# Optimization experiments

Measured on AMD Instinct MI355X. Metric: run time of the kernel, lower is better.

## Reference

```python
import jax, jax.numpy as jnp
import numpy as np

EMBED_DIM = 512
NUM_HEADS = 8
HEAD_DIM = EMBED_DIM // NUM_HEADS
PAIR_BONUS = 2.0
MIN_SEPARATION = 3
PAIRING_MATRIX = jnp.array([
    [0, 1, 0, 0, 0],
    [1, 0, 1, 0, 0],
    [0, 1, 0, 1, 0],
    [0, 0, 1, 0, 0],
    [0, 0, 0, 0, 0],
], dtype=jnp.float32)


def setup_inputs() -> dict:
    key = jax.random.key(0)
    ks = jax.random.split(key, 12)
    B, S, E = 8, 1024, EMBED_DIM
    scale = 1.0 / np.sqrt(E)
    inp = {
        "query": jax.random.normal(ks[0], (B, S, E), dtype=jnp.float32),
        "key": jax.random.normal(ks[1], (B, S, E), dtype=jnp.float32),
        "value": jax.random.normal(ks[2], (B, S, E), dtype=jnp.float32),
        "nucleotide_sequence": jax.random.randint(ks[3], (B, S), 0, 5, dtype=jnp.int32),
        "key_padding_mask": jnp.zeros((B, S), dtype=bool),
        "Wq": jax.random.normal(ks[4], (E, E), dtype=jnp.float32) * scale,
        "bq": jnp.zeros((E,), dtype=jnp.float32),
        "Wk": jax.random.normal(ks[5], (E, E), dtype=jnp.float32) * scale,
        "bk": jnp.zeros((E,), dtype=jnp.float32),
        "Wv": jax.random.normal(ks[6], (E, E), dtype=jnp.float32) * scale,
        "bv": jnp.zeros((E,), dtype=jnp.float32),
        "Wo": jax.random.normal(ks[7], (E, E), dtype=jnp.float32) * scale,
        "bo": jnp.zeros((E,), dtype=jnp.float32),
    }
    return inp


def reference(query, key, value, nucleotide_sequence, key_padding_mask,
              Wq, bq, Wk, bk, Wv, bv, Wo, bo):
    B, T, E = query.shape
    S = key.shape[1]
    H, D = NUM_HEADS, HEAD_DIM
    scaling = D ** -0.5

    # projections -> (B, H, L, D)
    q = (query @ Wq + bq).reshape(B, T, H, D).transpose(0, 2, 1, 3)
    k = (key @ Wk + bk).reshape(B, S, H, D).transpose(0, 2, 1, 3)
    v = (value @ Wv + bv).reshape(B, S, H, D).transpose(0, 2, 1, 3)

    attn = jnp.einsum('bhtd,bhsd->bhts', q, k) * scaling  # (B,H,T,S)

    # base-pairing bias: gather into 5x5 table, masked by min separation
    pos = jnp.arange(S)
    sep_ok = (jnp.abs(pos[:, None] - pos[None, :]) >= MIN_SEPARATION).astype(jnp.float32)
    pairing = PAIRING_MATRIX[nucleotide_sequence[:, :, None], nucleotide_sequence[:, None, :]]  # (B,S,S)
    pair_bonus = pairing * sep_ok[None] * PAIR_BONUS
    attn = attn + pair_bonus[:, None, :, :]

    # key padding mask -> -inf
    attn = jnp.where(key_padding_mask[:, None, None, :], -jnp.inf, attn)

    attn_probs = jax.nn.softmax(attn, axis=-1)
    out = jnp.einsum('bhts,bhsd->bhtd', attn_probs, v)
    out = out.transpose(0, 2, 1, 3).reshape(B, T, E)
    out = out @ Wo + bo
    return out, attn_probs
```

## Files before the change

kernel.cpp:

```cpp
#include <hip/hip_runtime.h>
#include <hip/hip_bf16.h>
#include <stdint.h>


typedef float  f32x4  __attribute__((ext_vector_type(4)));
typedef short  s16x8  __attribute__((ext_vector_type(8)));

__device__ __forceinline__ ushort f2bf(float f) {
  union { float f; uint32_t u; } v; v.f = f;
  uint32_t u = v.u;
  return (ushort)((u + 0x7FFF + ((u >> 16) & 1)) >> 16);
}

__device__ __forceinline__ f32x4 mfma16(s16x8 a, s16x8 b, f32x4 c) {
  return __builtin_amdgcn_mfma_f32_16x16x32_bf16(a, b, c, 0, 0, 0);
}

__device__ __forceinline__ void gl_lds16(const void* g, void* l) {
  typedef __attribute__((address_space(1))) const void gvoid;
  typedef __attribute__((address_space(3))) void lvoid;
  __builtin_amdgcn_global_load_lds((gvoid*)(uintptr_t)g,
                                   (lvoid*)(uint32_t)(uintptr_t)l, 16, 0, 0);
}

__device__ __forceinline__ void vwait4() {
  asm volatile("s_waitcnt vmcnt(4)" ::: "memory");
  __builtin_amdgcn_sched_barrier(0);
}
__device__ __forceinline__ void vwait2() {
  asm volatile("s_waitcnt vmcnt(2)" ::: "memory");
  __builtin_amdgcn_sched_barrier(0);
}
__device__ __forceinline__ void vwait0() {
  asm volatile("s_waitcnt vmcnt(0)" ::: "memory");
  __builtin_amdgcn_sched_barrier(0);
}
__device__ __forceinline__ void bar_lds() {
  asm volatile("s_waitcnt lgkmcnt(0)" ::: "memory");
  __builtin_amdgcn_s_barrier();
  __builtin_amdgcn_sched_barrier(0);
}

__global__ __launch_bounds__(256) void k_convert_w(
    const float* __restrict__ Wq, const float* __restrict__ Wk,
    const float* __restrict__ Wv, const float* __restrict__ Wo,
    ushort* __restrict__ WT, ushort* __restrict__ WoT) {
  int idx = blockIdx.x * 256 + threadIdx.x;
  int row = idx >> 9;
  int k = idx & 511;
  if (row < 1536) {
    const float* W = (row < 512) ? Wq : (row < 1024 ? Wk : Wv);
    int n = row & 511;
    WT[row * 512 + k] = f2bf(W[k * 512 + n]);
  } else {
    int n = row - 1536;
    WoT[n * 512 + k] = f2bf(Wo[k * 512 + n]);
  }
}

__global__ __launch_bounds__(256) void k_gemm_qkv(
    const float* __restrict__ Aq, const float* __restrict__ Ak,
    const float* __restrict__ Av, const ushort* __restrict__ WT,
    const float* __restrict__ bq, const float* __restrict__ bk,
    const float* __restrict__ bv, ushort* __restrict__ Y) {
  __shared__ ushort As[128 * 64];
  __shared__ ushort Bs[128 * 64];
  const int id = blockIdx.x;
  const int xcd = id & 7, slot = id >> 3;
  const int mb = xcd * 8 + slot / 12;
  const int nb = slot % 12;
  const int mat = nb >> 2;
  const float* A    = (mat == 0) ? Aq : (mat == 1 ? Ak : Av);
  const float* bias = (mat == 0) ? bq : (mat == 1 ? bk : bv);
  const int tid = threadIdx.x;
  const int w = tid >> 6, l = tid & 63;
  const int wr = (w >> 1) * 64, wc = (w & 1) * 64;
  const int lr = l & 15, lg = l >> 4;
  const int srow = l >> 3, sslot = (l & 7) ^ srow;

  f32x4 acc[4][4];
#pragma unroll
  for (int i = 0; i < 4; i++)
#pragma unroll
    for (int j = 0; j < 4; j++) acc[i][j] = (f32x4){0.f, 0.f, 0.f, 0.f};

  for (int kk = 0; kk < 8; kk++) {
    const int k0 = kk * 64;
#pragma unroll
    for (int it = 0; it < 8; it++) {
      int s2 = it * 256 + tid;
      int row = s2 >> 4;
      int k4 = (s2 & 15) * 4;
      float4 v = *reinterpret_cast<const float4*>(
          &A[(size_t)(mb * 128 + row) * 512 + k0 + k4]);
      uint64_t p = (uint64_t)f2bf(v.x) | ((uint64_t)f2bf(v.y) << 16) |
                   ((uint64_t)f2bf(v.z) << 32) | ((uint64_t)f2bf(v.w) << 48);
      int boff = row * 128 + ((k4 * 2) ^ ((row & 7) << 4));
      *reinterpret_cast<uint64_t*>((char*)As + boff) = p;
    }
#pragma unroll
    for (int it = 0; it < 4; it++) {
      int g8 = it * 4 + w;
      int row = g8 * 8 + srow;
      gl_lds16(&WT[(size_t)(nb * 128 + row) * 512 + k0 + sslot * 8], &Bs[g8 * 512]);
    }
    __syncthreads();
#pragma unroll
    for (int ks = 0; ks < 2; ks++) {
      s16x8 af[4], bfr[4];
#pragma unroll
      for (int mt = 0; mt < 4; mt++) {
        int row = wr + mt * 16 + lr;
        af[mt] = *reinterpret_cast<const s16x8*>(
            (char*)As + row * 128 + ((ks * 64 + lg * 16) ^ ((row & 7) << 4)));
      }
#pragma unroll
      for (int nt = 0; nt < 4; nt++) {
        int row = wc + nt * 16 + lr;
        bfr[nt] = *reinterpret_cast<const s16x8*>(
            (char*)Bs + row * 128 + ((ks * 64 + lg * 16) ^ ((row & 7) << 4)));
      }
#pragma unroll
      for (int mt = 0; mt < 4; mt++)
#pragma unroll
        for (int nt = 0; nt < 4; nt++)
          acc[mt][nt] = mfma16(af[mt], bfr[nt], acc[mt][nt]);
    }
    __syncthreads();
  }
  const int ncb = nb * 128;
#pragma unroll
  for (int nt = 0; nt < 4; nt++) {
    int gcol = ncb + wc + nt * 16 + lr;
    float bv_ = bias[gcol & 511];
#pragma unroll
    for (int mt = 0; mt < 4; mt++) {
#pragma unroll
      for (int r = 0; r < 4; r++) {
        int grow = mb * 128 + wr + mt * 16 + lg * 4 + r;
        Y[(size_t)grow * 1536 + gcol] = f2bf(acc[mt][nt][r] + bv_);
      }
    }
  }
}

__global__ __launch_bounds__(256) void k_transpose_v(
    const ushort* __restrict__ Y, ushort* __restrict__ vT) {
  __shared__ ushort T[64 * 64];
  const int sc = blockIdx.x;
  const int bh = blockIdx.y;
  const int b = bh >> 3, h = bh & 7;
  const int s0 = sc * 64;
  const int tid = threadIdx.x;
#pragma unroll
  for (int it = 0; it < 2; it++) {
    int slot = it * 256 + tid;
    int srw = slot >> 3;
    int i16 = (slot & 7) * 16;
    int4 v = *reinterpret_cast<const int4*>(
        &Y[(size_t)(b * 1024 + s0 + srw) * 1536 + 1024 + h * 64 + (slot & 7) * 8]);
    *reinterpret_cast<int4*>((char*)T + srw * 128 + (i16 ^ ((srw & 7) << 4))) = v;
  }
  __syncthreads();
  const int d = tid >> 2;
  const int sseg = (tid & 3) * 16;
  int pk[8];
#pragma unroll
  for (int j = 0; j < 8; j++) {
    int s0l = sseg + 2 * j;
    uint32_t a = *reinterpret_cast<const ushort*>(
        (char*)T + s0l * 128 + ((d * 2) ^ ((s0l & 7) << 4)));
    uint32_t bb = *reinterpret_cast<const ushort*>(
        (char*)T + (s0l + 1) * 128 + ((d * 2) ^ (((s0l + 1) & 7) << 4)));
    pk[j] = (int)(a | (bb << 16));
  }
  ushort* dst = &vT[(size_t)(bh * 64 + d) * 1024 + s0 + sseg];
  int4 o0 = {pk[0], pk[1], pk[2], pk[3]};
  int4 o1 = {pk[4], pk[5], pk[6], pk[7]};
  *reinterpret_cast<int4*>(dst) = o0;
  *reinterpret_cast<int4*>(dst + 8) = o1;
}

__global__ __launch_bounds__(256, 4) void k_attn_core(
    const ushort* __restrict__ Y, const ushort* __restrict__ vT,
    const int* __restrict__ seq, const unsigned char* __restrict__ mask,
    float* __restrict__ rinv_ws, ushort* __restrict__ AO) {
  __shared__ ushort Kb[2][4096];
  __shared__ ushort Vb[2][4096];
  __shared__ ushort Qb[1024];
  __shared__ ushort Pb[16 * 72];
  __shared__ ushort seqm[1024];
  __shared__ float rinv_s[16];
  float* Rbuf = reinterpret_cast<float*>(&Kb[0][0]);

  const int id = blockIdx.x;
  const int xcd = id & 7, slot = id >> 3;
  const int bh = xcd * 8 + (slot >> 6);
  const int tb = slot & 63;
  const int b = bh >> 3, h = bh & 7;
  const int tid = threadIdx.x;
  const int w = tid >> 6, l = tid & 63;
  const int lr = l & 15, lg = l >> 4;
  const int sc_ = w * 16;
  const int srw = sc_ + lr;
  const int srow = l >> 3, sslot = (l & 7) ^ srow;

#pragma unroll
  for (int it = 0; it < 4; it++) {
    int s = it * 256 + tid;
    seqm[s] = (ushort)(seq[b * 1024 + s] | (mask[b * 1024 + s] ? 0x100 : 0));
  }
#pragma unroll
  for (int it = 0; it < 2; it++) {
    int g8 = w * 2 + it;
    int row = g8 * 8 + srow;
    gl_lds16(&Y[(size_t)(b * 1024 + row) * 1536 + 512 + h * 64 + sslot * 8],
             &Kb[0][g8 * 512]);
    gl_lds16(&vT[(size_t)(bh * 64 + row) * 1024 + sslot * 8], &Vb[0][g8 * 512]);
  }
  if (w < 2) {
    gl_lds16(&Y[(size_t)(b * 1024 + tb * 16 + w * 8 + srow) * 1536 + h * 64 +
                sslot * 8],
             &Qb[w * 512]);
  }
  __syncthreads();

  s16x8 qf0 = *reinterpret_cast<const s16x8*>(
      (char*)Qb + lr * 128 + ((lg * 16) ^ ((lr & 7) << 4)));
  s16x8 qf1 = *reinterpret_cast<const s16x8*>(
      (char*)Qb + lr * 128 + ((64 + lg * 16) ^ ((lr & 7) << 4)));
  int seqt[4];
#pragma unroll
  for (int r = 0; r < 4; r++) seqt[r] = seqm[tb * 16 + lg * 4 + r] & 255;

  float psum[4] = {0.f, 0.f, 0.f, 0.f};
  f32x4 oacc = (f32x4){0.f, 0.f, 0.f, 0.f};

#pragma unroll
  for (int c = 0; c < 16; c++) {
    if (c < 15) {
#pragma unroll
      for (int it = 0; it < 2; it++) {
        int g8 = w * 2 + it;
        int row = g8 * 8 + srow;
        gl_lds16(&Y[(size_t)(b * 1024 + (c + 1) * 64 + row) * 1536 + 512 +
                    h * 64 + sslot * 8],
                 &Kb[(c + 1) & 1][g8 * 512]);
        gl_lds16(&vT[(size_t)(bh * 64 + row) * 1024 + (c + 1) * 64 + sslot * 8],
                 &Vb[(c + 1) & 1][g8 * 512]);
      }
      vwait4();
    } else {
      vwait0();
    }
    s16x8 kf0 = *reinterpret_cast<const s16x8*>(
        (char*)&Kb[c & 1][0] + srw * 128 + ((lg * 16) ^ ((srw & 7) << 4)));
    s16x8 kf1 = *reinterpret_cast<const s16x8*>(
        (char*)&Kb[c & 1][0] + srw * 128 + ((64 + lg * 16) ^ ((srw & 7) << 4)));
    f32x4 facc = (f32x4){0.f, 0.f, 0.f, 0.f};
    facc = mfma16(qf0, kf0, facc);
    facc = mfma16(qf1, kf1, facc);

    const int sg = c * 64 + srw;
    const int sm = seqm[sg];
    const int ss = sm & 255;
    const bool msk = (sm & 0x100) != 0;
#pragma unroll
    for (int r = 0; r < 4; r++) {
      int tg = tb * 16 + lg * 4 + r;
      int dsep = tg - sg; dsep = dsep < 0 ? -dsep : dsep;
      int dnt = seqt[r] - ss; dnt = dnt < 0 ? -dnt : dnt;
      bool bon = (dnt == 1 && seqt[r] <= 3 && ss <= 3 && dsep >= 3);
      float v = facc[r] * 0.125f + (bon ? 2.0f : 0.0f);
      float ee = msk ? 0.0f : __expf(v - 12.0f);
      psum[r] += ee;
      Pb[(lg * 4 + r) * 72 + srw] = f2bf(ee);
    }
    bar_lds();

#pragma unroll
    for (int ks = 0; ks < 2; ks++) {
      s16x8 paf = *reinterpret_cast<const s16x8*>(&Pb[lr * 72 + ks * 32 + lg * 8]);
      s16x8 vb = *reinterpret_cast<const s16x8*>(
          (char*)&Vb[c & 1][0] + srw * 128 +
          ((ks * 64 + lg * 16) ^ ((srw & 7) << 4)));
      oacc = mfma16(paf, vb, oacc);
    }
    bar_lds();
  }

#pragma unroll
  for (int r = 0; r < 4; r++) Rbuf[((w * 4 + lg) * 4 + r) * 16 + lr] = psum[r];
  __syncthreads();
  {
    int row = tid >> 4, j = tid & 15;
    int lgr = row >> 2, rr = row & 3;
    float s = 0.f;
#pragma unroll
    for (int i = 0; i < 4; i++) {
      int wj = j >> 2;
      int lrj = (j & 3) * 4 + i;
      s += Rbuf[((wj * 4 + lgr) * 4 + rr) * 16 + lrj];
    }
#pragma unroll
    for (int off = 1; off < 16; off <<= 1) s += __shfl_xor(s, off);
    if (j == 0) rinv_s[row] = 1.0f / s;
  }
  __syncthreads();
  if (tid < 16)
    rinv_ws[(size_t)bh * 1024 + tb * 16 + tid] = rinv_s[tid];
  float rv[4];
#pragma unroll
  for (int r = 0; r < 4; r++) rv[r] = rinv_s[lg * 4 + r];

#pragma unroll
  for (int r = 0; r < 4; r++) {
    int t = tb * 16 + lg * 4 + r;
    AO[((size_t)b * 1024 + t) * 512 + h * 64 + sc_ + lr] = f2bf(oacc[r] * rv[r]);
  }
}

__global__ __launch_bounds__(256, 8) void k_probs(
    const ushort* __restrict__ Y, const float* __restrict__ rinv_ws,
    const int* __restrict__ seq, const unsigned char* __restrict__ mask,
    float* __restrict__ probs) {
  __shared__ ushort Kb[2][4096];
  __shared__ ushort Qb[1024];
  __shared__ unsigned char seqm8[1024];

  const int id = blockIdx.x;
  const int xcd = id & 7, slot = id >> 3;
  const int bh = xcd * 8 + (slot >> 6);
  const int tb = slot & 63;
  const int b = bh >> 3, h = bh & 7;
  const int tid = threadIdx.x;
  const int w = tid >> 6, l = tid & 63;
  const int lr = l & 15, lg = l >> 4;
  const int srw = w * 16 + lr;
  const int srow = l >> 3, sslot = (l & 7) ^ srow;

#pragma unroll
  for (int it = 0; it < 4; it++) {
    int s = it * 256 + tid;
    seqm8[s] =
        (unsigned char)(seq[b * 1024 + s] | (mask[b * 1024 + s] ? 16 : 0));
  }
#pragma unroll
  for (int it = 0; it < 2; it++) {
    int g8 = w * 2 + it;
    int row = g8 * 8 + srow;
    gl_lds16(&Y[(size_t)(b * 1024 + row) * 1536 + 512 + h * 64 + sslot * 8],
             &Kb[0][g8 * 512]);
  }
  if (w < 2) {
    gl_lds16(&Y[(size_t)(b * 1024 + tb * 16 + w * 8 + srow) * 1536 + h * 64 +
                sslot * 8],
             &Qb[w * 512]);
  }
  __syncthreads();

  s16x8 qf0 = *reinterpret_cast<const s16x8*>(
      (char*)Qb + lr * 128 + ((lg * 16) ^ ((lr & 7) << 4)));
  s16x8 qf1 = *reinterpret_cast<const s16x8*>(
      (char*)Qb + lr * 128 + ((64 + lg * 16) ^ ((lr & 7) << 4)));
  int seqt[4];
  float rv[4];
  float* prow[4];
#pragma unroll
  for (int r = 0; r < 4; r++) {
    int t = tb * 16 + lg * 4 + r;
    seqt[r] = seqm8[t] & 15;
    rv[r] = rinv_ws[(size_t)bh * 1024 + t];
    prow[r] = &probs[((size_t)bh * 1024 + t) * 1024 + srw];
  }

#pragma unroll
  for (int c = 0; c < 16; c++) {
    if (c < 15) {
#pragma unroll
      for (int it = 0; it < 2; it++) {
        int g8 = w * 2 + it;
        int row = g8 * 8 + srow;
        gl_lds16(&Y[(size_t)(b * 1024 + (c + 1) * 64 + row) * 1536 + 512 +
                    h * 64 + sslot * 8],
                 &Kb[(c + 1) & 1][g8 * 512]);
      }
      vwait2();
    } else {
      vwait0();
    }
    s16x8 kf0 = *reinterpret_cast<const s16x8*>(
        (char*)&Kb[c & 1][0] + srw * 128 + ((lg * 16) ^ ((srw & 7) << 4)));
    s16x8 kf1 = *reinterpret_cast<const s16x8*>(
        (char*)&Kb[c & 1][0] + srw * 128 + ((64 + lg * 16) ^ ((srw & 7) << 4)));
    f32x4 facc = (f32x4){0.f, 0.f, 0.f, 0.f};
    facc = mfma16(qf0, kf0, facc);
    facc = mfma16(qf1, kf1, facc);

    const int sg = c * 64 + srw;
    const int sm = seqm8[sg];
    const int ss = sm & 15;
    const bool msk = (sm & 16) != 0;
#pragma unroll
    for (int r = 0; r < 4; r++) {
      int tg = tb * 16 + lg * 4 + r;
      int dsep = tg - sg; dsep = dsep < 0 ? -dsep : dsep;
      int dnt = seqt[r] - ss; dnt = dnt < 0 ? -dnt : dnt;
      bool bon = (dnt == 1 && seqt[r] <= 3 && ss <= 3 && dsep >= 3);
      float v = facc[r] * 0.125f + (bon ? 2.0f : 0.0f);
      float ee = msk ? 0.0f : __expf(v - 12.0f);
      __builtin_nontemporal_store(ee * rv[r], prow[r] + c * 64);
    }
  }
}

__global__ __launch_bounds__(256) void k_gemm_o(
    const ushort* __restrict__ AO, const ushort* __restrict__ WoT,
    const float* __restrict__ bo, float* __restrict__ out) {
  __shared__ ushort As[128 * 64];
  __shared__ ushort Bs[128 * 64];
  const int id = blockIdx.x;
  const int xcd = id & 7, slot = id >> 3;
  const int mb = xcd * 8 + (slot >> 2);
  const int nb = slot & 3;
  const int tid = threadIdx.x;
  const int w = tid >> 6, l = tid & 63;
  const int wr = (w >> 1) * 64, wc = (w & 1) * 64;
  const int lr = l & 15, lg = l >> 4;
  const int srow = l >> 3, sslot = (l & 7) ^ srow;

  f32x4 acc[4][4];
#pragma unroll
  for (int i = 0; i < 4; i++)
#pragma unroll
    for (int j = 0; j < 4; j++) acc[i][j] = (f32x4){0.f, 0.f, 0.f, 0.f};

  for (int kk = 0; kk < 8; kk++) {
    const int k0 = kk * 64;
#pragma unroll
    for (int it = 0; it < 4; it++) {
      int g8 = it * 4 + w;
      int row = g8 * 8 + srow;
      gl_lds16(&AO[(size_t)(mb * 128 + row) * 512 + k0 + sslot * 8], &As[g8 * 512]);
      gl_lds16(&WoT[(size_t)(nb * 128 + row) * 512 + k0 + sslot * 8], &Bs[g8 * 512]);
    }
    __syncthreads();
#pragma unroll
    for (int ks = 0; ks < 2; ks++) {
      s16x8 af[4], bfr[4];
#pragma unroll
      for (int mt = 0; mt < 4; mt++) {
        int row = wr + mt * 16 + lr;
        af[mt] = *reinterpret_cast<const s16x8*>(
            (char*)As + row * 128 + ((ks * 64 + lg * 16) ^ ((row & 7) << 4)));
      }
#pragma unroll
      for (int nt = 0; nt < 4; nt++) {
        int row = wc + nt * 16 + lr;
        bfr[nt] = *reinterpret_cast<const s16x8*>(
            (char*)Bs + row * 128 + ((ks * 64 + lg * 16) ^ ((row & 7) << 4)));
      }
#pragma unroll
      for (int mt = 0; mt < 4; mt++)
#pragma unroll
        for (int nt = 0; nt < 4; nt++)
          acc[mt][nt] = mfma16(af[mt], bfr[nt], acc[mt][nt]);
    }
    __syncthreads();
  }
  const int ncb = nb * 128;
#pragma unroll
  for (int nt = 0; nt < 4; nt++) {
    int gcol = ncb + wc + nt * 16 + lr;
    float bv_ = bo[gcol];
#pragma unroll
    for (int mt = 0; mt < 4; mt++) {
#pragma unroll
      for (int r = 0; r < 4; r++) {
        int grow = mb * 128 + wr + mt * 16 + lg * 4 + r;
        out[(size_t)grow * 512 + gcol] = acc[mt][nt][r] + bv_;
      }
    }
  }
}

extern "C" void kernel_launch(void* const* d_in, const int* in_sizes, int n_in,
                              void* d_out, int out_size, void* d_ws, size_t ws_size,
                              hipStream_t stream) {
  (void)in_sizes; (void)n_in; (void)out_size; (void)ws_size;
  const float* query = (const float*)d_in[0];
  const float* key   = (const float*)d_in[1];
  const float* value = (const float*)d_in[2];
  const int* seq     = (const int*)d_in[3];
  const unsigned char* mask = (const unsigned char*)d_in[4];
  const float* Wq = (const float*)d_in[5];
  const float* bq = (const float*)d_in[6];
  const float* Wk = (const float*)d_in[7];
  const float* bk = (const float*)d_in[8];
  const float* Wv = (const float*)d_in[9];
  const float* bv = (const float*)d_in[10];
  const float* Wo = (const float*)d_in[11];
  const float* bo = (const float*)d_in[12];

  float* out = (float*)d_out;
  float* probs = out + (size_t)8 * 1024 * 512;

  char* ws = (char*)d_ws;
  ushort* Y      = (ushort*)(ws);
  ushort* WT     = (ushort*)(ws + 25165824);
  ushort* WoT    = (ushort*)(ws + 26738688);
  ushort* vT     = (ushort*)(ws + 27262976);
  ushort* AO     = (ushort*)(ws + 35651584);
  float*  rinv_ws= (float*)(ws + 44040192);

  k_convert_w<<<4096, 256, 0, stream>>>(Wq, Wk, Wv, Wo, WT, WoT);
  k_gemm_qkv<<<768, 256, 0, stream>>>(query, key, value, WT, bq, bk, bv, Y);
  k_transpose_v<<<dim3(16, 64), 256, 0, stream>>>(Y, vT);
  k_attn_core<<<4096, 256, 0, stream>>>(Y, vT, seq, mask, rinv_ws, AO);
  k_probs<<<4096, 256, 0, stream>>>(Y, rinv_ws, seq, mask, probs);
  k_gemm_o<<<256, 256, 0, stream>>>(AO, WoT, bo, out);
}
```

Before: 226.8 us.

## Transpose probs MFMA so each lane stores contiguous float4 rows, buffering in bf16

The operands of the QK MFMA are swapped in the probs kernel so each lane holds four consecutive key columns for a single query row. This lets the kernel emit 16-byte vectorized nontemporal stores in place of scattered scalar stores. The exponentials for all 16 chunks are held in registers as packed bf16 and written out at the end. That packing rounds the probabilities to bf16 precision, and occupancy is lowered from 8 to 6 blocks to make room for the extra registers.

```diff
diff --git a/kernel.cpp b/kernel.cpp
--- a/kernel.cpp
+++ b/kernel.cpp
@@ -10,6 +10,11 @@
   union { float f; uint32_t u; } v; v.f = f;
   uint32_t u = v.u;
   return (ushort)((u + 0x7FFF + ((u >> 16) & 1)) >> 16);
+}
+
+__device__ __forceinline__ float bf2f(uint32_t u) {
+  union { uint32_t u; float f; } v; v.u = u << 16;
+  return v.f;
 }
 
 __device__ __forceinline__ f32x4 mfma16(s16x8 a, s16x8 b, f32x4 c) {
@@ -320,7 +325,7 @@
   }
 }
 
-__global__ __launch_bounds__(256, 8) void k_probs(
+__global__ __launch_bounds__(256, 6) void k_probs(
     const ushort* __restrict__ Y, const float* __restrict__ rinv_ws,
     const int* __restrict__ seq, const unsigned char* __restrict__ mask,
     float* __restrict__ probs) {
@@ -363,16 +368,13 @@
       (char*)Qb + lr * 128 + ((lg * 16) ^ ((lr & 7) << 4)));
   s16x8 qf1 = *reinterpret_cast<const s16x8*>(
       (char*)Qb + lr * 128 + ((64 + lg * 16) ^ ((lr & 7) << 4)));
-  int seqt[4];
-  float rv[4];
-  float* prow[4];
-#pragma unroll
-  for (int r = 0; r < 4; r++) {
-    int t = tb * 16 + lg * 4 + r;
-    seqt[r] = seqm8[t] & 15;
-    rv[r] = rinv_ws[(size_t)bh * 1024 + t];
-    prow[r] = &probs[((size_t)bh * 1024 + t) * 1024 + srw];
-  }
+
+  const int t_ = tb * 16 + lr;
+  const int st_ = seqm8[t_] & 15;
+  const float rv_ = rinv_ws[(size_t)bh * 1024 + t_];
+  const int sloc = w * 16 + lg * 4;
+
+  uint2 pe[16];
 
 #pragma unroll
   for (int c = 0; c < 16; c++) {
@@ -394,23 +396,39 @@
     s16x8 kf1 = *reinterpret_cast<const s16x8*>(
         (char*)&Kb[c & 1][0] + srw * 128 + ((64 + lg * 16) ^ ((srw & 7) << 4)));
     f32x4 facc = (f32x4){0.f, 0.f, 0.f, 0.f};
-    facc = mfma16(qf0, kf0, facc);
-    facc = mfma16(qf1, kf1, facc);
-
-    const int sg = c * 64 + srw;
-    const int sm = seqm8[sg];
-    const int ss = sm & 15;
-    const bool msk = (sm & 16) != 0;
+    facc = mfma16(kf0, qf0, facc);
+    facc = mfma16(kf1, qf1, facc);
+
+    const int sbase = c * 64 + sloc;
+    const uint32_t sm4 =
+        *reinterpret_cast<const uint32_t*>(&seqm8[sbase]);
+    ushort eb[4];
 #pragma unroll
     for (int r = 0; r < 4; r++) {
-      int tg = tb * 16 + lg * 4 + r;
-      int dsep = tg - sg; dsep = dsep < 0 ? -dsep : dsep;
-      int dnt = seqt[r] - ss; dnt = dnt < 0 ? -dnt : dnt;
-      bool bon = (dnt == 1 && seqt[r] <= 3 && ss <= 3 && dsep >= 3);
+      const int sgr = sbase + r;
+      const int smb = (sm4 >> (8 * r)) & 0xff;
+      const int ss = smb & 15;
+      const bool msk = (smb & 16) != 0;
+      int dsep = t_ - sgr; dsep = dsep < 0 ? -dsep : dsep;
+      int dnt = st_ - ss; dnt = dnt < 0 ? -dnt : dnt;
+      bool bon = (dnt == 1 && st_ <= 3 && ss <= 3 && dsep >= 3);
       float v = facc[r] * 0.125f + (bon ? 2.0f : 0.0f);
       float ee = msk ? 0.0f : __expf(v - 12.0f);
-      __builtin_nontemporal_store(ee * rv[r], prow[r] + c * 64);
-    }
+      eb[r] = f2bf(ee);
+    }
+    pe[c].x = (uint32_t)eb[0] | ((uint32_t)eb[1] << 16);
+    pe[c].y = (uint32_t)eb[2] | ((uint32_t)eb[3] << 16);
+  }
+
+  float* prow_ = &probs[((size_t)bh * 1024 + t_) * 1024 + sloc];
+#pragma unroll
+  for (int c = 0; c < 16; c++) {
+    f32x4 o;
+    o.x = bf2f(pe[c].x & 0xffffu) * rv_;
+    o.y = bf2f(pe[c].x >> 16) * rv_;
+    o.z = bf2f(pe[c].y & 0xffffu) * rv_;
+    o.w = bf2f(pe[c].y >> 16) * rv_;
+    __builtin_nontemporal_store(o, reinterpret_cast<f32x4*>(prow_ + c * 64));
   }
 }
 
```

Result: slower. 249.3 us (+9.9%).
